# Performance work log

Measured on AMD Instinct MI355X. Metric: run time of the kernel, lower is better.

The kernel has to match this reference:

```python
import jax, jax.numpy as jnp
import numpy as np

NUM_CLASSES = 6
STYLE_DIM = 64
NUM_POINTS = 1000
EMBED_DIM = 1024
NUM_ADAPTERS = 256
LN_EPS = 1e-5


def setup_inputs() -> dict:
    key = jax.random.key(0)
    ks = jax.random.split(key, 24)
    B, N = 8, 64
    ef = jax.random.normal(ks[0], (B, N, EMBED_DIM), dtype=jnp.float32)
    class_labels = jax.random.randint(ks[1], (B, N), 0, NUM_CLASSES)
    adapter_ids = jax.random.randint(ks[2], (B, N), 0, NUM_ADAPTERS)

    def lin(k, fan_in, fan_out):
        lim = 1.0 / np.sqrt(fan_in)
        kw, kb = jax.random.split(k)
        w = jax.random.uniform(kw, (fan_in, fan_out), minval=-lim, maxval=lim, dtype=jnp.float32)
        b = jax.random.uniform(kb, (fan_out,), minval=-lim, maxval=lim, dtype=jnp.float32)
        return w, b

    # StyleEncoder: Linear(1024,256), LayerNorm(256), ReLU, Linear(256,64)
    se_w1, se_b1 = lin(ks[3], EMBED_DIM, 256)
    se_gamma = jnp.ones((256,), jnp.float32)
    se_beta = jnp.zeros((256,), jnp.float32)
    se_w2, se_b2 = lin(ks[4], 256, STYLE_DIM)

    # GlobalEntityPrior MLP: (style+3+classes) -> 256 -> 256 -> 19
    in_dim = STYLE_DIM + 3 + NUM_CLASSES
    gep_w1, gep_b1 = lin(ks[5], in_dim, 256)
    gep_w2, gep_b2 = lin(ks[6], 256, 256)
    gep_w3, gep_b3 = lin(ks[7], 256, 19)
    canonical_points = jax.random.normal(ks[8], (NUM_POINTS, 3), dtype=jnp.float32)

    # LocalResidualAdapter tables (torch init is zeros; use small randn for nontrivial test)
    mu_tab = 0.02 * jax.random.normal(ks[9], (NUM_ADAPTERS, NUM_POINTS, 3), dtype=jnp.float32)
    cov_tab = 0.02 * jax.random.normal(ks[10], (NUM_ADAPTERS, NUM_POINTS, 6), dtype=jnp.float32)
    op_tab = 0.02 * jax.random.normal(ks[11], (NUM_ADAPTERS, NUM_POINTS, 1), dtype=jnp.float32)
    sh_tab = 0.02 * jax.random.normal(ks[12], (NUM_ADAPTERS, NUM_POINTS, 9), dtype=jnp.float32)

    return {
        "entity_features": ef, "class_labels": class_labels, "adapter_ids": adapter_ids,
        "se_w1": se_w1, "se_b1": se_b1, "se_gamma": se_gamma, "se_beta": se_beta,
        "se_w2": se_w2, "se_b2": se_b2,
        "canonical_points": canonical_points,
        "gep_w1": gep_w1, "gep_b1": gep_b1, "gep_w2": gep_w2, "gep_b2": gep_b2,
        "gep_w3": gep_w3, "gep_b3": gep_b3,
        "mu_tab": mu_tab, "cov_tab": cov_tab, "op_tab": op_tab, "sh_tab": sh_tab,
    }


def reference(entity_features, class_labels, adapter_ids,
              se_w1, se_b1, se_gamma, se_beta, se_w2, se_b2,
              canonical_points, gep_w1, gep_b1, gep_w2, gep_b2, gep_w3, gep_b3,
              mu_tab, cov_tab, op_tab, sh_tab):
    # --- StyleEncoder ---
    h = entity_features @ se_w1 + se_b1                       # (B,N,256)
    mean = jnp.mean(h, axis=-1, keepdims=True)
    var = jnp.mean((h - mean) ** 2, axis=-1, keepdims=True)
    h = (h - mean) * jax.lax.rsqrt(var + LN_EPS) * se_gamma + se_beta
    h = jax.nn.relu(h)
    style = h @ se_w2 + se_b2                                 # (B,N,style_dim)

    # --- GlobalEntityPrior: first layer decomposed over concat [style, points, onehot] ---
    oh = jax.nn.one_hot(class_labels, NUM_CLASSES, dtype=jnp.float32)  # (B,N,C)
    w_s = gep_w1[:STYLE_DIM]                                  # (style_dim,256)
    w_p = gep_w1[STYLE_DIM:STYLE_DIM + 3]                     # (3,256)
    w_c = gep_w1[STYLE_DIM + 3:]                              # (C,256)
    ent_part = style @ w_s + oh @ w_c + gep_b1                # (B,N,256)
    pt_part = canonical_points @ w_p                          # (P,256)
    h1 = jax.nn.relu(ent_part[:, :, None, :] + pt_part[None, None])  # (B,N,P,256)
    h2 = jax.nn.relu(h1 @ gep_w2 + gep_b2)                    # (B,N,P,256)
    params = h2 @ gep_w3 + gep_b3                             # (B,N,P,19)

    p_mu = params[..., 0:3]
    p_cov = params[..., 3:9]
    p_op = jax.nn.sigmoid(params[..., 9:10])
    p_sh = params[..., 10:]

    # --- LocalResidualAdapter gather (replaces python dict loop) ---
    final_mu = p_mu + mu_tab[adapter_ids]                     # (B,N,P,3)
    final_cov = p_cov + cov_tab[adapter_ids]                  # (B,N,P,6)
    final_op = p_op + op_tab[adapter_ids]                     # (B,N,P,1)
    final_sh = p_sh + sh_tab[adapter_ids]                     # (B,N,P,9)
    return (final_mu, final_cov, final_op, final_sh)
```

## Files before the change

kernel.cpp:

```cpp
#include <hip/hip_runtime.h>

typedef __attribute__((ext_vector_type(8))) short short8;
typedef __attribute__((ext_vector_type(4))) float float4v;
typedef __attribute__((ext_vector_type(16))) float float16v;

#define SDIM 64

#define MU_OFF   0
#define COV_OFF  1536000
#define OP_OFF   4608000
#define SH_OFF   5120000

__device__ __forceinline__ float bf2f(unsigned short u){ return __uint_as_float(((unsigned)u)<<16); }
__device__ __forceinline__ unsigned short f2bf(float f){
  unsigned u = __float_as_uint(f);
  return (unsigned short)((u + 0x7fffu + ((u>>16)&1u)) >> 16);
}
__device__ __forceinline__ unsigned cvt_pk_bf16(float lo, float hi){
  unsigned r; asm("v_cvt_pk_bf16_f32 %0, %1, %2" : "=v"(r) : "v"(lo), "v"(hi)); return r;
}

__global__ __launch_bounds__(256) void kprep(
    const float* __restrict__ se_w1, const float* __restrict__ gep_w2,
    const float* __restrict__ gep_w3, const float* __restrict__ gep_w1,
    const float* __restrict__ cpts,
    unsigned short* __restrict__ w1b, unsigned short* __restrict__ w2t,
    unsigned short* __restrict__ w3p, unsigned short* __restrict__ ptb){
  int idx = blockIdx.x*256 + threadIdx.x;
  if (idx < 262144){ w1b[idx] = f2bf(se_w1[idx]); return; }
  int i1 = idx - 262144;
  if (i1 < 65536){ int n = i1 >> 8, k = i1 & 255; w2t[i1] = f2bf(gep_w2[k*256+n]); return; }
  int i2 = idx - 327680;
  if (i2 < 8192){ int j = i2 >> 8, k = i2 & 255; w3p[i2] = f2bf(j < 19 ? gep_w3[k*19+j] : 0.f); return; }
  int i3 = idx - 335872;
  if (i3 < 256000){ int p = i3 >> 8, k = i3 & 255;
    float v = cpts[p*3+0]*gep_w1[(SDIM+0)*256+k]
            + cpts[p*3+1]*gep_w1[(SDIM+1)*256+k]
            + cpts[p*3+2]*gep_w1[(SDIM+2)*256+k];
    ptb[i3] = f2bf(v);
  }
}

__global__ __launch_bounds__(512, 2) void kmain(
    const float* __restrict__ ef, const int* __restrict__ cls_lab,
    const unsigned short* __restrict__ w1b,
    const float* __restrict__ se_b1, const float* __restrict__ se_gamma,
    const float* __restrict__ se_beta, const float* __restrict__ se_w2,
    const float* __restrict__ se_b2,
    const float* __restrict__ gep_w1, const float* __restrict__ gep_b1,
    const unsigned short* __restrict__ ptb, const unsigned short* __restrict__ w2t,
    const unsigned short* __restrict__ w3p,
    const float* __restrict__ gep_b2, const float* __restrict__ gep_b3,
    const int* __restrict__ adapter_ids,
    const float* __restrict__ mu_tab, const float* __restrict__ cov_tab,
    const float* __restrict__ op_tab, const float* __restrict__ sh_tab,
    float* __restrict__ out){
  __shared__ unsigned short h1L[64*256];
  __shared__ unsigned short w3L[32*256];
  __shared__ float entL[256];
  __shared__ float b2L[256];
  __shared__ float b3L[32];
  __shared__ float pL[2][64][21];
  int e = blockIdx.x, t = threadIdx.x;
  int lane = t & 63, wid = t >> 6;
  int l16 = lane & 15, kq = lane >> 4;

  {
    float* efF = (float*)h1L;
    float* red = (float*)h1L + 1024;
    float* scr = (float*)w3L;
    ((float2*)efF)[t] = ((const float2*)(ef + (size_t)e*1024))[t];
    if (t < 256) b2L[t] = gep_b2[t];
    if (t < 32) b3L[t] = (t < 19) ? gep_b3[t] : 0.f;
    __syncthreads();
    {
      int kg = t >> 5, c8 = (t & 31)*8;
      const unsigned short* wrow = w1b + (kg*64)*256 + c8;
      float a[8];
      #pragma unroll
      for (int j=0;j<8;j++) a[j]=0.f;
      #pragma unroll 8
      for (int k=0;k<64;k++){
        short8 w = *(const short8*)(wrow + k*256);
        float ev = efF[kg*64 + k];
        #pragma unroll
        for (int j=0;j<8;j++) a[j] += ev * bf2f((unsigned short)w[j]);
      }
      #pragma unroll
      for (int j=0;j<8;j++) red[kg*256 + c8 + j] = a[j];
    }
    __syncthreads();
    float h = 0.f;
    if (t < 256){
      float s = 0.f;
      #pragma unroll
      for (int g=0; g<16; g++) s += red[g*256 + t];
      h = s + se_b1[t];
    }
    float s1 = h, s2 = h*h;
    #pragma unroll
    for (int o=32;o>0;o>>=1){ s1 += __shfl_xor(s1,o,64); s2 += __shfl_xor(s2,o,64); }
    if (lane==0){ scr[1344+wid]=s1; scr[1352+wid]=s2; }
    __syncthreads();
    float S1=0.f, S2=0.f;
    #pragma unroll
    for (int i=0;i<8;i++){ S1 += scr[1344+i]; S2 += scr[1352+i]; }
    float mean = S1*(1.f/256.f);
    float var  = S2*(1.f/256.f) - mean*mean;
    if (t < 256){
      float hn = (h-mean)*rsqrtf(var+1e-5f)*se_gamma[t] + se_beta[t];
      scr[512+t] = fmaxf(hn, 0.f);
    }
    __syncthreads();
    {
      int s = t & 63, q = t >> 6;
      float st = 0.f;
      #pragma unroll 4
      for (int k=q*32;k<q*32+32;k++) st += scr[512+k]*se_w2[k*64+s];
      scr[768 + q*64 + s] = st;
    }
    __syncthreads();
    if (t < 64){
      float v = 0.f;
      #pragma unroll
      for (int q=0;q<8;q++) v += scr[768 + q*64 + t];
      scr[1280+t] = v + se_b2[t];
    }
    __syncthreads();
    if (t < 256){
      int c = cls_lab[e];
      float ep = gep_b1[t] + gep_w1[(SDIM+3+c)*256 + t];
      #pragma unroll 8
      for (int k=0;k<64;k++) ep += scr[1280+k]*gep_w1[k*256+t];
      entL[t] = ep;
    }
    __syncthreads();
  }

  #pragma unroll
  for (int i=0;i<2;i++){
    int g = t + i*512; int row = g>>5; int kg = g&31;
    uint4 v = *(const uint4*)(w3p + row*256 + kg*8);
    int bo = (row*512 + kg*16) ^ ((row&7)<<4);
    *(uint4*)((char*)w3L + bo) = v;
  }
  short8 bB[8][2];
  #pragma unroll
  for (int s=0;s<8;s++)
    #pragma unroll
    for (int r=0;r<2;r++){
      int n  = wid*32 + r*16 + l16;
      int k0 = s*32 + kq*8;
      bB[s][r] = *(const short8*)(w2t + n*256 + k0);
    }
  __syncthreads();

  int aid = adapter_ids[e];
  const float* muT  = mu_tab  + (size_t)aid*3000;
  const float* covT = cov_tab + (size_t)aid*6000;
  const float* opT  = op_tab  + (size_t)aid*1000;
  const float* shT  = sh_tab  + (size_t)aid*9000;
  int kg0 = (t & 31)*8;

  uint4 pv[4];
  #pragma unroll
  for (int i=0;i<4;i++){
    int p = (t>>5) + i*16;
    pv[i] = *(const uint4*)(ptb + p*256 + (t&31)*8);
  }

  float tmu=0.f, tcov=0.f, top=0.f, tsh0=0.f, tsh1=0.f;

  for (int c=0;c<16;c++){
    int p0 = c*64;
    {
      float4v e0 = *(float4v*)&entL[kg0];
      float4v e1 = *(float4v*)&entL[kg0+4];
      #pragma unroll
      for (int i=0;i<4;i++){
        int row = (t>>5) + i*16;
        unsigned pw[4] = {pv[i].x, pv[i].y, pv[i].z, pv[i].w};
        unsigned rw[4];
        #pragma unroll
        for (int w=0; w<4; w++){
          float er0 = (w<2)? e0[2*w]   : e1[2*w-4];
          float er1 = (w<2)? e0[2*w+1] : e1[2*w-3];
          float lo = __uint_as_float(pw[w]<<16);
          float hi = __uint_as_float(pw[w] & 0xffff0000u);
          lo = fmaxf(lo + er0, 0.f); hi = fmaxf(hi + er1, 0.f);
          rw[w] = cvt_pk_bf16(lo, hi);
        }
        int bo = (row*512 + (t&31)*16) ^ ((row&7)<<4);
        *(uint4*)((char*)h1L + bo) = make_uint4(rw[0],rw[1],rw[2],rw[3]);
      }
    }
    if (c > 0 && t >= 128){
      int tt = t - 128;
      int g0 = (c-1)*64;
      if (tt < 192) tmu  = muT [g0*3 + tt];
      if (tt < 384) tcov = covT[g0*6 + tt];
      if (tt < 64)  top  = opT [g0 + tt];
      if (tt < 384) tsh0 = shT [g0*9 + tt];
      if (tt < 192) tsh1 = shT [g0*9 + 384 + tt];
    }
    __syncthreads();
    {
      int p0n = p0 + 64;
      #pragma unroll
      for (int i=0;i<4;i++){
        int p = p0n + (t>>5) + i*16; p = (p>999)?999:p;
        pv[i] = *(const uint4*)(ptb + p*256 + (t&31)*8);
      }
    }
    float4v acc[4][2];
    #pragma unroll
    for (int m=0;m<4;m++){
      acc[m][0] = (float4v){0.f,0.f,0.f,0.f};
      acc[m][1] = (float4v){0.f,0.f,0.f,0.f};
    }
    #pragma unroll
    for (int s=0;s<8;s++){
      #pragma unroll
      for (int m=0;m<4;m++){
        int row = m*16 + l16;
        int bo = (row*512 + s*64 + kq*16) ^ ((row&7)<<4);
        short8 a = *(const short8*)((char*)h1L + bo);
        acc[m][0] = __builtin_amdgcn_mfma_f32_16x16x32_bf16(bB[s][0], a, acc[m][0], 0,0,0);
        acc[m][1] = __builtin_amdgcn_mfma_f32_16x16x32_bf16(bB[s][1], a, acc[m][1], 0,0,0);
      }
    }
    __syncthreads();
    {
      float4v bias0 = *(float4v*)&b2L[wid*32 + kq*4];
      float4v bias1 = *(float4v*)&b2L[wid*32 + 16 + kq*4];
      #pragma unroll
      for (int m=0;m<4;m++){
        int p = m*16 + l16;
        int rowx = (p&7)<<4;
        #pragma unroll
        for (int r=0;r<2;r++){
          float4v b = r ? bias1 : bias0;
          float v0 = fmaxf(acc[m][r][0]+b[0], 0.f);
          float v1 = fmaxf(acc[m][r][1]+b[1], 0.f);
          float v2 = fmaxf(acc[m][r][2]+b[2], 0.f);
          float v3 = fmaxf(acc[m][r][3]+b[3], 0.f);
          unsigned w0 = cvt_pk_bf16(v0,v1);
          unsigned w1 = cvt_pk_bf16(v2,v3);
          int nbase = wid*32 + r*16 + kq*4;
          int bo = (p*512 + nbase*2) ^ rowx;
          uint2 val; val.x = w0; val.y = w1;
          *(uint2*)((char*)h1L + bo) = val;
        }
      }
    }
    __syncthreads();
    if (wid < 2){
      float16v acc2;
      #pragma unroll
      for (int r=0;r<16;r++) acc2[r] = 0.f;
      int pr = wid*32 + (lane & 31);
      int jr = lane & 31;
      int kb2 = (lane >> 5) * 16;
      int prx = (pr&7)<<4, jrx = (jr&7)<<4;
      #pragma unroll
      for (int s=0;s<16;s++){
        int nb = s*32 + kb2;
        short8 a2 = *(const short8*)((char*)h1L + ((pr*512 + nb) ^ prx));
        short8 bw = *(const short8*)((char*)w3L + ((jr*512 + nb) ^ jrx));
        acc2 = __builtin_amdgcn_mfma_f32_32x32x16_bf16(a2, bw, acc2, 0,0,0);
      }
      if (jr < 19){
        float bj = b3L[jr];
        int pb = wid*32 + 4*(lane>>5);
        #pragma unroll
        for (int r=0;r<16;r++){
          int p_out = pb + (r&3) + 8*(r>>2);
          pL[c&1][p_out][jr] = acc2[r] + bj;
        }
      }
    } else if (c > 0){
      int tt = t - 128;
      int par = (c-1)&1;
      int base = e*1000 + (c-1)*64;
      if (tt < 192){ int p=tt/3, q=tt-p*3; out[MU_OFF + base*3 + tt] = pL[par][p][q] + tmu; }
      if (tt < 384){ int p=tt/6, q=tt-p*6; out[COV_OFF + base*6 + tt] = pL[par][p][3+q] + tcov; }
      if (tt < 64){ float v = pL[par][tt][9]; out[OP_OFF + base + tt] = 1.f/(1.f+__expf(-v)) + top; }
      if (tt < 384){ int p=tt/9, q=tt-p*9; out[SH_OFF + base*9 + tt] = pL[par][p][10+q] + tsh0; }
      if (tt < 192){ int i2=tt+384; int p=i2/9, q=i2-p*9; out[SH_OFF + base*9 + i2] = pL[par][p][10+q] + tsh1; }
    }
    __syncthreads();
  }
  {
    int base = e*1000 + 960;
    float gmu=0.f,gcov=0.f,gop=0.f,gsh=0.f;
    if (t < 120) gmu  = muT [2880 + t];
    if (t < 240) gcov = covT[5760 + t];
    if (t < 40)  gop  = opT [960 + t];
    if (t < 360) gsh  = shT [8640 + t];
    if (t < 120){ int p=t/3, q=t-p*3; out[MU_OFF + base*3 + t] = pL[1][p][q] + gmu; }
    if (t < 240){ int p=t/6, q=t-p*6; out[COV_OFF + base*6 + t] = pL[1][p][3+q] + gcov; }
    if (t < 40){ float v = pL[1][t][9]; out[OP_OFF + base + t] = 1.f/(1.f+__expf(-v)) + gop; }
    if (t < 360){ int p=t/9, q=t-p*9; out[SH_OFF + base*9 + t] = pL[1][p][10+q] + gsh; }
  }
}

extern "C" void kernel_launch(void* const* d_in, const int* in_sizes, int n_in,
                              void* d_out, int out_size, void* d_ws, size_t ws_size,
                              hipStream_t stream){
  const float* ef    = (const float*)d_in[0];
  const int*   cls   = (const int*)d_in[1];
  const int*   aid   = (const int*)d_in[2];
  const float* se_w1 = (const float*)d_in[3];
  const float* se_b1 = (const float*)d_in[4];
  const float* se_g  = (const float*)d_in[5];
  const float* se_be = (const float*)d_in[6];
  const float* se_w2 = (const float*)d_in[7];
  const float* se_b2 = (const float*)d_in[8];
  const float* cpts  = (const float*)d_in[9];
  const float* gw1   = (const float*)d_in[10];
  const float* gb1   = (const float*)d_in[11];
  const float* gw2   = (const float*)d_in[12];
  const float* gb2   = (const float*)d_in[13];
  const float* gw3   = (const float*)d_in[14];
  const float* gb3   = (const float*)d_in[15];
  const float* mu_t  = (const float*)d_in[16];
  const float* cov_t = (const float*)d_in[17];
  const float* op_t  = (const float*)d_in[18];
  const float* sh_t  = (const float*)d_in[19];
  float* out = (float*)d_out;
  char* ws = (char*)d_ws;
  unsigned short* w1b = (unsigned short*)(ws);
  unsigned short* w2t = (unsigned short*)(ws + 524288);
  unsigned short* w3p = (unsigned short*)(ws + 655360);
  unsigned short* ptb = (unsigned short*)(ws + 671744);

  kprep<<<2312, 256, 0, stream>>>(se_w1, gw2, gw3, gw1, cpts, w1b, w2t, w3p, ptb);
  kmain<<<512, 512, 0, stream>>>(ef, cls, w1b, se_b1, se_g, se_be, se_w2, se_b2,
                                 gw1, gb1, ptb, w2t, w3p, gb2, gb3, aid,
                                 mu_t, cov_t, op_t, sh_t, out);
}
```

Measured before the change: 139.0 us.

## Use 32x32x16 MFMA for layer-2 GEMM and split h1/h2 staging into halves

The second MLP layer now uses 32x32x16 bf16 MFMAs instead of 16x16x32, with each wave holding 16 weight fragments and computing two 32-row point halves in sequence. The h1 build and the h2 write-back are each split around extra barriers, so the first half's GEMM can start while the second half of h1 is still being written, and h2 is written in place half by half. The entity-bias loads are also hoisted out of the chunk loop. The aim is higher matrix-core efficiency and some overlap, at the cost of one more barrier per chunk and a different accumulator layout.

```diff
diff --git a/kernel.cpp b/kernel.cpp
--- a/kernel.cpp
+++ b/kernel.cpp
@@ -63,7 +63,8 @@
   __shared__ float pL[2][64][21];
   int e = blockIdx.x, t = threadIdx.x;
   int lane = t & 63, wid = t >> 6;
-  int l16 = lane & 15, kq = lane >> 4;
+  int l16 = lane & 15;
+  int l32 = lane & 31, hi = lane >> 5;
 
   {
     float* efF = (float*)h1L;
@@ -144,15 +145,10 @@
     int bo = (row*512 + kg*16) ^ ((row&7)<<4);
     *(uint4*)((char*)w3L + bo) = v;
   }
-  short8 bB[8][2];
+  short8 bB[16];
   #pragma unroll
-  for (int s=0;s<8;s++)
-    #pragma unroll
-    for (int r=0;r<2;r++){
-      int n  = wid*32 + r*16 + l16;
-      int k0 = s*32 + kq*8;
-      bB[s][r] = *(const short8*)(w2t + n*256 + k0);
-    }
+  for (int s=0;s<16;s++)
+    bB[s] = *(const short8*)(w2t + (wid*32 + l32)*256 + s*16 + hi*8);
   __syncthreads();
 
   int aid = adapter_ids[e];
@@ -161,6 +157,8 @@
   const float* opT  = op_tab  + (size_t)aid*1000;
   const float* shT  = sh_tab  + (size_t)aid*9000;
   int kg0 = (t & 31)*8;
+  float4v e0 = *(float4v*)&entL[kg0];
+  float4v e1 = *(float4v*)&entL[kg0+4];
 
   uint4 pv[4];
   #pragma unroll
@@ -173,26 +171,40 @@
 
   for (int c=0;c<16;c++){
     int p0 = c*64;
-    {
-      float4v e0 = *(float4v*)&entL[kg0];
-      float4v e1 = *(float4v*)&entL[kg0+4];
-      #pragma unroll
-      for (int i=0;i<4;i++){
-        int row = (t>>5) + i*16;
-        unsigned pw[4] = {pv[i].x, pv[i].y, pv[i].z, pv[i].w};
-        unsigned rw[4];
-        #pragma unroll
-        for (int w=0; w<4; w++){
-          float er0 = (w<2)? e0[2*w]   : e1[2*w-4];
-          float er1 = (w<2)? e0[2*w+1] : e1[2*w-3];
-          float lo = __uint_as_float(pw[w]<<16);
-          float hi = __uint_as_float(pw[w] & 0xffff0000u);
-          lo = fmaxf(lo + er0, 0.f); hi = fmaxf(hi + er1, 0.f);
-          rw[w] = cvt_pk_bf16(lo, hi);
-        }
-        int bo = (row*512 + (t&31)*16) ^ ((row&7)<<4);
-        *(uint4*)((char*)h1L + bo) = make_uint4(rw[0],rw[1],rw[2],rw[3]);
-      }
+    #pragma unroll
+    for (int i=0;i<2;i++){
+      int row = (t>>5) + i*16;
+      unsigned pw[4] = {pv[i].x, pv[i].y, pv[i].z, pv[i].w};
+      unsigned rw[4];
+      #pragma unroll
+      for (int w=0; w<4; w++){
+        float er0 = (w<2)? e0[2*w]   : e1[2*w-4];
+        float er1 = (w<2)? e0[2*w+1] : e1[2*w-3];
+        float lo = __uint_as_float(pw[w]<<16);
+        float hi2 = __uint_as_float(pw[w] & 0xffff0000u);
+        lo = fmaxf(lo + er0, 0.f); hi2 = fmaxf(hi2 + er1, 0.f);
+        rw[w] = cvt_pk_bf16(lo, hi2);
+      }
+      int bo = (row*512 + (t&31)*16) ^ ((row&7)<<4);
+      *(uint4*)((char*)h1L + bo) = make_uint4(rw[0],rw[1],rw[2],rw[3]);
+    }
+    __syncthreads();
+    #pragma unroll
+    for (int i=2;i<4;i++){
+      int row = (t>>5) + i*16;
+      unsigned pw[4] = {pv[i].x, pv[i].y, pv[i].z, pv[i].w};
+      unsigned rw[4];
+      #pragma unroll
+      for (int w=0; w<4; w++){
+        float er0 = (w<2)? e0[2*w]   : e1[2*w-4];
+        float er1 = (w<2)? e0[2*w+1] : e1[2*w-3];
+        float lo = __uint_as_float(pw[w]<<16);
+        float hi2 = __uint_as_float(pw[w] & 0xffff0000u);
+        lo = fmaxf(lo + er0, 0.f); hi2 = fmaxf(hi2 + er1, 0.f);
+        rw[w] = cvt_pk_bf16(lo, hi2);
+      }
+      int bo = (row*512 + (t&31)*16) ^ ((row&7)<<4);
+      *(uint4*)((char*)h1L + bo) = make_uint4(rw[0],rw[1],rw[2],rw[3]);
     }
     if (c > 0 && t >= 128){
       int tt = t - 128;
@@ -203,7 +215,6 @@
       if (tt < 384) tsh0 = shT [g0*9 + tt];
       if (tt < 192) tsh1 = shT [g0*9 + 384 + tt];
     }
-    __syncthreads();
     {
       int p0n = p0 + 64;
       #pragma unroll
@@ -212,45 +223,58 @@
         pv[i] = *(const uint4*)(ptb + p*256 + (t&31)*8);
       }
     }
-    float4v acc[4][2];
-    #pragma unroll
-    for (int m=0;m<4;m++){
-      acc[m][0] = (float4v){0.f,0.f,0.f,0.f};
-      acc[m][1] = (float4v){0.f,0.f,0.f,0.f};
-    }
-    #pragma unroll
-    for (int s=0;s<8;s++){
-      #pragma unroll
-      for (int m=0;m<4;m++){
-        int row = m*16 + l16;
-        int bo = (row*512 + s*64 + kq*16) ^ ((row&7)<<4);
-        short8 a = *(const short8*)((char*)h1L + bo);
-        acc[m][0] = __builtin_amdgcn_mfma_f32_16x16x32_bf16(bB[s][0], a, acc[m][0], 0,0,0);
-        acc[m][1] = __builtin_amdgcn_mfma_f32_16x16x32_bf16(bB[s][1], a, acc[m][1], 0,0,0);
-      }
-    }
-    __syncthreads();
-    {
-      float4v bias0 = *(float4v*)&b2L[wid*32 + kq*4];
-      float4v bias1 = *(float4v*)&b2L[wid*32 + 16 + kq*4];
-      #pragma unroll
-      for (int m=0;m<4;m++){
-        int p = m*16 + l16;
-        int rowx = (p&7)<<4;
-        #pragma unroll
-        for (int r=0;r<2;r++){
-          float4v b = r ? bias1 : bias0;
-          float v0 = fmaxf(acc[m][r][0]+b[0], 0.f);
-          float v1 = fmaxf(acc[m][r][1]+b[1], 0.f);
-          float v2 = fmaxf(acc[m][r][2]+b[2], 0.f);
-          float v3 = fmaxf(acc[m][r][3]+b[3], 0.f);
-          unsigned w0 = cvt_pk_bf16(v0,v1);
-          unsigned w1 = cvt_pk_bf16(v2,v3);
-          int nbase = wid*32 + r*16 + kq*4;
-          int bo = (p*512 + nbase*2) ^ rowx;
-          uint2 val; val.x = w0; val.y = w1;
-          *(uint2*)((char*)h1L + bo) = val;
-        }
+    float16v acc0, acc1;
+    #pragma unroll
+    for (int r=0;r<16;r++){ acc0[r] = 0.f; acc1[r] = 0.f; }
+    {
+      int prx = (l32&7)<<4;
+      int kb = hi*16;
+      #pragma unroll
+      for (int s=0;s<16;s++){
+        short8 b = *(const short8*)((char*)h1L + ((l32*512 + s*32 + kb) ^ prx));
+        acc0 = __builtin_amdgcn_mfma_f32_32x32x16_bf16(bB[s], b, acc0, 0,0,0);
+      }
+    }
+    __syncthreads();
+    {
+      int pr = 32 + l32;
+      int prx = (pr&7)<<4;
+      int kb = hi*16;
+      #pragma unroll
+      for (int s=0;s<16;s++){
+        short8 b = *(const short8*)((char*)h1L + ((pr*512 + s*32 + kb) ^ prx));
+        acc1 = __builtin_amdgcn_mfma_f32_32x32x16_bf16(bB[s], b, acc1, 0,0,0);
+      }
+    }
+    {
+      int p = l32;
+      int rowx = (p&7)<<4;
+      #pragma unroll
+      for (int run=0; run<4; run++){
+        int nb = wid*32 + run*8 + hi*4;
+        float4v bz = *(float4v*)&b2L[nb];
+        float v0 = fmaxf(acc0[run*4+0]+bz[0], 0.f);
+        float v1 = fmaxf(acc0[run*4+1]+bz[1], 0.f);
+        float v2 = fmaxf(acc0[run*4+2]+bz[2], 0.f);
+        float v3 = fmaxf(acc0[run*4+3]+bz[3], 0.f);
+        uint2 val; val.x = cvt_pk_bf16(v0,v1); val.y = cvt_pk_bf16(v2,v3);
+        *(uint2*)((char*)h1L + ((p*512 + nb*2) ^ rowx)) = val;
+      }
+    }
+    __syncthreads();
+    {
+      int p = 32 + l32;
+      int rowx = (p&7)<<4;
+      #pragma unroll
+      for (int run=0; run<4; run++){
+        int nb = wid*32 + run*8 + hi*4;
+        float4v bz = *(float4v*)&b2L[nb];
+        float v0 = fmaxf(acc1[run*4+0]+bz[0], 0.f);
+        float v1 = fmaxf(acc1[run*4+1]+bz[1], 0.f);
+        float v2 = fmaxf(acc1[run*4+2]+bz[2], 0.f);
+        float v3 = fmaxf(acc1[run*4+3]+bz[3], 0.f);
+        uint2 val; val.x = cvt_pk_bf16(v0,v1); val.y = cvt_pk_bf16(v2,v3);
+        *(uint2*)((char*)h1L + ((p*512 + nb*2) ^ rowx)) = val;
       }
     }
     __syncthreads();
@@ -258,9 +282,9 @@
       float16v acc2;
       #pragma unroll
       for (int r=0;r<16;r++) acc2[r] = 0.f;
-      int pr = wid*32 + (lane & 31);
-      int jr = lane & 31;
-      int kb2 = (lane >> 5) * 16;
+      int pr = wid*32 + l32;
+      int jr = l32;
+      int kb2 = hi * 16;
       int prx = (pr&7)<<4, jrx = (jr&7)<<4;
       #pragma unroll
       for (int s=0;s<16;s++){
@@ -271,7 +295,7 @@
       }
       if (jr < 19){
         float bj = b3L[jr];
-        int pb = wid*32 + 4*(lane>>5);
+        int pb = wid*32 + 4*hi;
         #pragma unroll
         for (int r=0;r<16;r++){
           int p_out = pb + (r&3) + 8*(r>>2);
```

After: 134.4 us. 1.03x faster.
